# Kernel optimization log

Measured on AMD Instinct MI355X. Metric: run time of the kernel, lower is better.

Reference implementation:

```python
import jax, jax.numpy as jnp
import numpy as np

B, N, S = 8, 512, 96
SD = TD = H = 256
NH, HD = 8, 32  # num_heads, head_dim
OUT = 4


def setup_inputs() -> dict:
    key = jax.random.key(0)
    ks = jax.random.split(key, 20)
    g = lambda k, shape: (jax.random.normal(k, shape, dtype=jnp.float32) * 0.02)
    return {
        "spatial_features": jax.random.normal(ks[0], (B, N, SD), dtype=jnp.float32),
        "temporal_features": jax.random.normal(ks[1], (B, S, TD), dtype=jnp.float32),
        "Ws": g(ks[2], (H, SD)),   "bs": g(ks[3], (H,)),
        "Wt": g(ks[4], (H, TD)),   "bt": g(ks[5], (H,)),
        "Win": g(ks[6], (3 * H, H)), "bin": g(ks[7], (3 * H,)),
        "Wao": g(ks[8], (H, H)),   "bao": g(ks[9], (H,)),
        "W1": g(ks[10], (H, H)),   "b1": g(ks[11], (H,)),
        "Wo1": g(ks[12], (H // 2, H)), "bo1": g(ks[13], (H // 2,)),
        "Wo2": g(ks[14], (OUT, H // 2)), "bo2": g(ks[15], (OUT,)),
    }


def reference(spatial_features, temporal_features, Ws, bs, Wt, bt, Win, bin, Wao, bao,
              W1, b1, Wo1, bo1, Wo2, bo2):
    # Projections
    sp = spatial_features @ Ws.T + bs          # [B, N, H]
    tp = temporal_features @ Wt.T + bt         # [B, S, H]
    # MultiheadAttention in_proj (batched over all N node-queries at once;
    # mathematically identical to the original per-node loop)
    Wq, Wk, Wv = Win[:H], Win[H:2 * H], Win[2 * H:]
    bq, bk, bv = bin[:H], bin[H:2 * H], bin[2 * H:]
    q = (sp @ Wq.T + bq).reshape(B, N, NH, HD)   # [B, N, h, d]
    k = (tp @ Wk.T + bk).reshape(B, S, NH, HD)   # [B, S, h, d]
    v = (tp @ Wv.T + bv).reshape(B, S, NH, HD)
    scale = 1.0 / np.sqrt(HD).astype(np.float32)
    logits = jnp.einsum('bnhd,bshd->bhns', q * scale, k)   # [B, h, N, S]
    attn = jax.nn.softmax(logits, axis=-1)
    ctx = jnp.einsum('bhns,bshd->bnhd', attn, v).reshape(B, N, H)
    attended = ctx @ Wao.T + bao               # [B, N, H] (out_proj)
    # fusion_layer: Linear + ReLU (dropout=identity in eval)
    fused = jax.nn.relu(attended @ W1.T + b1)  # [B, N, H]
    # output_layer: Linear -> ReLU -> Linear
    h2 = jax.nn.relu(fused @ Wo1.T + bo1)      # [B, N, H/2]
    y = h2 @ Wo2.T + bo2                       # [B, N, OUT]
    # original expands over seq_len BEFORE fusion_layer; since all layers are
    # pointwise over the (S, N) grid, compute once per node and broadcast.
    return jnp.broadcast_to(y[:, None, :, :], (B, S, N, OUT))
```

## Files before the change

### kernel.cpp

```cpp
#include <hip/hip_runtime.h>

#define BB 8
#define NN 512
#define SS 96
#define HH 256
#define NHD 8
#define HDD 32
#define OUTD 4

#define Q_OFF   0
#define K_OFF   (4096*256)
#define V_OFF   (K_OFF + 768*256)
#define CTX_OFF (V_OFF + 768*256)
#define BF_BASE (CTX_OFF + 4096*256)
#define WSB_OFF  0
#define WTB_OFF  65536
#define WINB_OFF 131072
#define WAOB_OFF 327680
#define W1B_OFF  393216
#define WO1B_OFF 458752
#define BF_TOTAL 491520

typedef __attribute__((ext_vector_type(8))) short bf16x8;
typedef __attribute__((ext_vector_type(4))) float f32x4;

__device__ __forceinline__ unsigned short f2bf(float f) {
    unsigned int u = __float_as_uint(f);
    u = (u + 0x7FFFu + ((u >> 16) & 1u)) >> 16;
    return (unsigned short)u;
}

__global__ __launch_bounds__(256) void k_cast(
    const float* __restrict__ Ws, const float* __restrict__ Wt,
    const float* __restrict__ Win, const float* __restrict__ Wao,
    const float* __restrict__ W1, const float* __restrict__ Wo1,
    unsigned short* __restrict__ dst)
{
    int idx = blockIdx.x * 256 + threadIdx.x;
    for (int j4 = idx; j4 < BF_TOTAL / 4; j4 += 120 * 256) {
        int e = j4 * 4;
        const float* src; int off;
        if (e < 65536)       { src = Ws;  off = e; }
        else if (e < 131072) { src = Wt;  off = e - 65536; }
        else if (e < 327680) { src = Win; off = e - 131072; }
        else if (e < 393216) { src = Wao; off = e - 327680; }
        else if (e < 458752) { src = W1;  off = e - 393216; }
        else                 { src = Wo1; off = e - 458752; }
        float4 v = *(const float4*)(src + off);
        ushort4 o;
        o.x = f2bf(v.x); o.y = f2bf(v.y); o.z = f2bf(v.z); o.w = f2bf(v.w);
        *(ushort4*)(dst + e) = o;
    }
}

template<int NCT>
__device__ __forceinline__ void mfma_stage(
    const unsigned short* __restrict__ Asw,
    const unsigned short* __restrict__ Wb,
    int lane, int wave, f32x4 acc[NCT])
{
    const int row = lane & 15, kq = lane >> 4;
    #pragma unroll
    for (int ct = 0; ct < NCT; ++ct) acc[ct] = (f32x4){0.f, 0.f, 0.f, 0.f};
    #pragma unroll 2
    for (int kt = 0; kt < 8; ++kt) {
        const int slot = kt * 4 + kq;
        bf16x8 a = *(const bf16x8*)(Asw + row * 256 + ((slot ^ (row & 7)) << 3));
        #pragma unroll
        for (int ct = 0; ct < NCT; ++ct) {
            const unsigned short* wp =
                Wb + (size_t)((wave * NCT + ct) * 16 + row) * 256 + kt * 32 + kq * 8;
            bf16x8 b = *(const bf16x8*)wp;
            acc[ct] = __builtin_amdgcn_mfma_f32_16x16x32_bf16(a, b, acc[ct], 0, 0, 0);
        }
    }
}

template<int NCT, bool RELU>
__device__ __forceinline__ void epi_lds(
    unsigned short* __restrict__ OutSw, const float* __restrict__ bias,
    int lane, int wave, const f32x4 acc[NCT])
{
    const int col0 = lane & 15, rq = lane >> 4;
    #pragma unroll
    for (int ct = 0; ct < NCT; ++ct) {
        const int C = wave * NCT * 16 + ct * 16 + col0;
        const float bb = bias[C];
        const int slot = C >> 3, within = C & 7;
        #pragma unroll
        for (int r = 0; r < 4; ++r) {
            const int R = rq * 4 + r;
            float v = acc[ct][r] + bb;
            if (RELU) v = fmaxf(v, 0.f);
            OutSw[R * 256 + ((slot ^ (R & 7)) << 3) + within] = f2bf(v);
        }
    }
}

template<int NCT>
__device__ __forceinline__ void epi_global(
    float* __restrict__ Og, const float* __restrict__ bias,
    int lane, int wave, const f32x4 acc[NCT])
{
    const int col0 = lane & 15, rq = lane >> 4;
    #pragma unroll
    for (int ct = 0; ct < NCT; ++ct) {
        const int C = wave * NCT * 16 + ct * 16 + col0;
        const float bb = bias[C];
        #pragma unroll
        for (int r = 0; r < 4; ++r) {
            const int R = rq * 4 + r;
            Og[(size_t)R * 256 + C] = acc[ct][r] + bb;
        }
    }
}

__device__ __forceinline__ void stage_A(
    const float* __restrict__ Ag, unsigned short* __restrict__ Asw, int tid)
{
    #pragma unroll
    for (int ii = 0; ii < 4; ++ii) {
        int i = tid + ii * 256;
        int row = i >> 6, c4 = i & 63;
        float4 v = ((const float4*)(Ag + (size_t)row * 256))[c4];
        int col = c4 * 4;
        int slot = col >> 3, half = (col >> 2) & 1;
        ushort4 o;
        o.x = f2bf(v.x); o.y = f2bf(v.y); o.z = f2bf(v.z); o.w = f2bf(v.w);
        *(ushort4*)(Asw + row * 256 + ((slot ^ (row & 7)) << 3) + half * 4) = o;
    }
}

__global__ __launch_bounds__(256) void k_proj(
    const float* __restrict__ spatial, const float* __restrict__ temporal,
    const float* __restrict__ bs, const float* __restrict__ bt,
    const float* __restrict__ bin,
    const unsigned short* __restrict__ bfw,
    float* __restrict__ q_out, float* __restrict__ k_out, float* __restrict__ v_out)
{
    __shared__ __align__(16) unsigned short A0[16 * 256];
    __shared__ __align__(16) unsigned short MID[16 * 256];
    const int tid = threadIdx.x, lane = tid & 63, wave = tid >> 6;
    f32x4 acc[4];

    if (blockIdx.x < 256) {
        const int r0 = blockIdx.x * 16;
        stage_A(spatial + (size_t)r0 * 256, A0, tid);
        __syncthreads();
        mfma_stage<4>(A0, bfw + WSB_OFF, lane, wave, acc);
        epi_lds<4, false>(MID, bs, lane, wave, acc);
        __syncthreads();
        mfma_stage<4>(MID, bfw + WINB_OFF, lane, wave, acc);
        epi_global<4>(q_out + (size_t)r0 * 256, bin, lane, wave, acc);
    } else {
        const int r0 = (blockIdx.x - 256) * 16;
        stage_A(temporal + (size_t)r0 * 256, A0, tid);
        __syncthreads();
        mfma_stage<4>(A0, bfw + WTB_OFF, lane, wave, acc);
        epi_lds<4, false>(MID, bt, lane, wave, acc);
        __syncthreads();
        mfma_stage<4>(MID, bfw + WINB_OFF + 65536, lane, wave, acc);
        epi_global<4>(k_out + (size_t)r0 * 256, bin + 256, lane, wave, acc);
        mfma_stage<4>(MID, bfw + WINB_OFF + 131072, lane, wave, acc);
        epi_global<4>(v_out + (size_t)r0 * 256, bin + 512, lane, wave, acc);
    }
}

__global__ __launch_bounds__(256) void k_attn(
    const float* __restrict__ qg, const float* __restrict__ kg,
    const float* __restrict__ vg, float* __restrict__ ctxg)
{
    __shared__ __align__(16) float kl[SS][HDD];
    __shared__ __align__(16) float vl[SS][HDD];
    const int tid = threadIdx.x;
    const int blk = blockIdx.x;
    const int cc = blk & 3;
    const int h = (blk >> 2) & (NHD - 1);
    const int b = blk >> 5;

    for (int i = tid; i < SS * HDD / 4; i += 256) {
        int s = i >> 3, d4 = i & 7;
        ((float4*)kl[s])[d4] = *(const float4*)(kg + (size_t)(b * SS + s) * HH + h * HDD + d4 * 4);
        ((float4*)vl[s])[d4] = *(const float4*)(vg + (size_t)(b * SS + s) * HH + h * HDD + d4 * 4);
    }
    __syncthreads();

    const int hf = tid & 1;
    const int r = tid >> 1;
    const int n = cc * 128 + r;
    const float4* q4 = (const float4*)(qg + (size_t)(b * NN + n) * HH + h * HDD);
    float4 q[8];
    #pragma unroll
    for (int i = 0; i < 8; ++i) q[i] = q4[i];

    const float scale = 0.17677669529663687f;
    float sum = 0.f;
    float4 ctx[8] = {};
    const int s0 = hf * 48;
    for (int s = s0; s < s0 + 48; ++s) {
        float dot = 0.f;
        #pragma unroll
        for (int i = 0; i < 8; ++i) {
            float4 kk = ((const float4*)kl[s])[i];
            dot += q[i].x * kk.x + q[i].y * kk.y + q[i].z * kk.z + q[i].w * kk.w;
        }
        float p = __expf(dot * scale);
        sum += p;
        #pragma unroll
        for (int i = 0; i < 8; ++i) {
            float4 vv = ((const float4*)vl[s])[i];
            ctx[i].x += p * vv.x; ctx[i].y += p * vv.y;
            ctx[i].z += p * vv.z; ctx[i].w += p * vv.w;
        }
    }
    sum += __shfl_xor(sum, 1);
    #pragma unroll
    for (int i = 0; i < 8; ++i) {
        ctx[i].x += __shfl_xor(ctx[i].x, 1);
        ctx[i].y += __shfl_xor(ctx[i].y, 1);
        ctx[i].z += __shfl_xor(ctx[i].z, 1);
        ctx[i].w += __shfl_xor(ctx[i].w, 1);
    }
    float inv = 1.0f / sum;
    float4* o4 = (float4*)(ctxg + (size_t)(b * NN + n) * HH + h * HDD);
    #pragma unroll
    for (int i = 0; i < 4; ++i) {
        int idx = hf * 4 + i;
        o4[idx] = make_float4(ctx[idx].x * inv, ctx[idx].y * inv,
                              ctx[idx].z * inv, ctx[idx].w * inv);
    }
}

__global__ __launch_bounds__(256) void k_head(
    const float* __restrict__ ctxg,
    const float* __restrict__ bao, const float* __restrict__ b1,
    const float* __restrict__ bo1,
    const float* __restrict__ Wo2, const float* __restrict__ bo2,
    const unsigned short* __restrict__ bfw,
    float* __restrict__ out)
{
    __shared__ __align__(16) unsigned short A0[16 * 256];
    __shared__ __align__(16) unsigned short MID[16 * 256];
    __shared__ __align__(16) float H2[16 * 128];
    __shared__ __align__(16) float y[16][OUTD];
    const int tid = threadIdx.x, lane = tid & 63, wave = tid >> 6;
    const int r0 = blockIdx.x * 16;
    f32x4 acc[4];

    stage_A(ctxg + (size_t)r0 * 256, A0, tid);
    __syncthreads();
    mfma_stage<4>(A0, bfw + WAOB_OFF, lane, wave, acc);
    epi_lds<4, false>(MID, bao, lane, wave, acc);
    __syncthreads();
    mfma_stage<4>(MID, bfw + W1B_OFF, lane, wave, acc);
    epi_lds<4, true>(A0, b1, lane, wave, acc);
    __syncthreads();
    {
        f32x4 a2[2];
        mfma_stage<2>(A0, bfw + WO1B_OFF, lane, wave, a2);
        const int col0 = lane & 15, rq = lane >> 4;
        #pragma unroll
        for (int ct = 0; ct < 2; ++ct) {
            const int C = wave * 32 + ct * 16 + col0;
            const float bb = bo1[C];
            #pragma unroll
            for (int r = 0; r < 4; ++r) {
                const int R = rq * 4 + r;
                H2[R * 128 + C] = fmaxf(a2[ct][r] + bb, 0.f);
            }
        }
    }
    __syncthreads();
    if (tid < 64) {
        int r = tid >> 2, o = tid & 3;
        float a = 0.f;
        const float4* w4 = (const float4*)(Wo2 + (size_t)o * 128);
        const float4* h4 = (const float4*)(H2 + r * 128);
        for (int kk = 0; kk < 32; ++kk) {
            float4 w = w4[kk], hv = h4[kk];
            a += hv.x * w.x + hv.y * w.y + hv.z * w.z + hv.w * w.w;
        }
        y[r][o] = a + bo2[o];
    }
    __syncthreads();
    const int b = r0 >> 9;
    const int nbase = r0 & 511;
    for (int i = tid; i < 16 * SS; i += 256) {
        int s = i >> 4;
        int r = i & 15;
        *(float4*)(out + ((size_t)(b * SS + s) * NN + (nbase + r)) * OUTD) = *(const float4*)y[r];
    }
}

extern "C" void kernel_launch(void* const* d_in, const int* in_sizes, int n_in,
                              void* d_out, int out_size, void* d_ws, size_t ws_size,
                              hipStream_t stream) {
    const float* spatial  = (const float*)d_in[0];
    const float* temporal = (const float*)d_in[1];
    const float* Ws  = (const float*)d_in[2];
    const float* bs  = (const float*)d_in[3];
    const float* Wt  = (const float*)d_in[4];
    const float* bt  = (const float*)d_in[5];
    const float* Win = (const float*)d_in[6];
    const float* bin = (const float*)d_in[7];
    const float* Wao = (const float*)d_in[8];
    const float* bao = (const float*)d_in[9];
    const float* W1  = (const float*)d_in[10];
    const float* b1  = (const float*)d_in[11];
    const float* Wo1 = (const float*)d_in[12];
    const float* bo1 = (const float*)d_in[13];
    const float* Wo2 = (const float*)d_in[14];
    const float* bo2 = (const float*)d_in[15];
    float* out = (float*)d_out;
    float* ws  = (float*)d_ws;

    float* qbuf   = ws + Q_OFF;
    float* kbuf   = ws + K_OFF;
    float* vbuf   = ws + V_OFF;
    float* ctxbuf = ws + CTX_OFF;
    unsigned short* bfw = (unsigned short*)(ws + BF_BASE);

    hipLaunchKernelGGL(k_cast, dim3(120), dim3(256), 0, stream,
                       Ws, Wt, Win, Wao, W1, Wo1, bfw);
    hipLaunchKernelGGL(k_proj, dim3(304), dim3(256), 0, stream,
                       spatial, temporal, bs, bt, bin, bfw, qbuf, kbuf, vbuf);
    hipLaunchKernelGGL(k_attn, dim3(BB * NHD * 4), dim3(256), 0, stream,
                       qbuf, kbuf, vbuf, ctxbuf);
    hipLaunchKernelGGL(k_head, dim3(BB * NN / 16), dim3(256), 0, stream,
                       ctxbuf, bao, b1, bo1, Wo2, bo2, bfw, out);
}
```

Baseline: 152.1 us.

## Fuse attention into head kernel with bf16 MFMA and bf16 Q/K/V^T buffers

Q, K and a transposed V are now stored as bf16 instead of fp32. The scalar fp32 attention kernel is replaced by MFMA-based logits and P·V computed inside the head kernel, so the context never goes to global memory and one launch is removed. This cuts memory traffic and moves the attention math onto the matrix cores. In exchange, probabilities and context are rounded to bf16, which costs some accuracy. Each block now handles all heads for 16 nodes, and the grid drops to 256 blocks.

```diff
diff --git a/kernel.cpp b/kernel.cpp
--- a/kernel.cpp
+++ b/kernel.cpp
@@ -8,11 +8,6 @@
 #define HDD 32
 #define OUTD 4
 
-#define Q_OFF   0
-#define K_OFF   (4096*256)
-#define V_OFF   (K_OFF + 768*256)
-#define CTX_OFF (V_OFF + 768*256)
-#define BF_BASE (CTX_OFF + 4096*256)
 #define WSB_OFF  0
 #define WTB_OFF  65536
 #define WINB_OFF 131072
@@ -20,6 +15,9 @@
 #define W1B_OFF  393216
 #define WO1B_OFF 458752
 #define BF_TOTAL 491520
+#define QB_OFF   491520
+#define KB_OFF   (QB_OFF + 1048576)
+#define VTB_OFF  (KB_OFF + 196608)
 
 typedef __attribute__((ext_vector_type(8))) short bf16x8;
 typedef __attribute__((ext_vector_type(4))) float f32x4;
@@ -98,8 +96,8 @@
 }
 
 template<int NCT>
-__device__ __forceinline__ void epi_global(
-    float* __restrict__ Og, const float* __restrict__ bias,
+__device__ __forceinline__ void epi_gbf16(
+    unsigned short* __restrict__ Og, const float* __restrict__ bias,
     int lane, int wave, const f32x4 acc[NCT])
 {
     const int col0 = lane & 15, rq = lane >> 4;
@@ -110,7 +108,7 @@
         #pragma unroll
         for (int r = 0; r < 4; ++r) {
             const int R = rq * 4 + r;
-            Og[(size_t)R * 256 + C] = acc[ct][r] + bb;
+            Og[(size_t)R * 256 + C] = f2bf(acc[ct][r] + bb);
         }
     }
 }
@@ -131,12 +129,13 @@
     }
 }
 
-__global__ __launch_bounds__(256) void k_proj(
+__global__ __launch_bounds__(256) void k_qkv(
     const float* __restrict__ spatial, const float* __restrict__ temporal,
     const float* __restrict__ bs, const float* __restrict__ bt,
     const float* __restrict__ bin,
     const unsigned short* __restrict__ bfw,
-    float* __restrict__ q_out, float* __restrict__ k_out, float* __restrict__ v_out)
+    unsigned short* __restrict__ qb, unsigned short* __restrict__ kb,
+    unsigned short* __restrict__ vtb)
 {
     __shared__ __align__(16) unsigned short A0[16 * 256];
     __shared__ __align__(16) unsigned short MID[16 * 256];
@@ -151,7 +150,7 @@
         epi_lds<4, false>(MID, bs, lane, wave, acc);
         __syncthreads();
         mfma_stage<4>(MID, bfw + WINB_OFF, lane, wave, acc);
-        epi_global<4>(q_out + (size_t)r0 * 256, bin, lane, wave, acc);
+        epi_gbf16<4>(qb + (size_t)r0 * 256, bin, lane, wave, acc);
     } else {
         const int r0 = (blockIdx.x - 256) * 16;
         stage_A(temporal + (size_t)r0 * 256, A0, tid);
@@ -160,95 +159,100 @@
         epi_lds<4, false>(MID, bt, lane, wave, acc);
         __syncthreads();
         mfma_stage<4>(MID, bfw + WINB_OFF + 65536, lane, wave, acc);
-        epi_global<4>(k_out + (size_t)r0 * 256, bin + 256, lane, wave, acc);
+        epi_gbf16<4>(kb + (size_t)r0 * 256, bin + 256, lane, wave, acc);
         mfma_stage<4>(MID, bfw + WINB_OFF + 131072, lane, wave, acc);
-        epi_global<4>(v_out + (size_t)r0 * 256, bin + 512, lane, wave, acc);
-    }
-}
-
-__global__ __launch_bounds__(256) void k_attn(
-    const float* __restrict__ qg, const float* __restrict__ kg,
-    const float* __restrict__ vg, float* __restrict__ ctxg)
-{
-    __shared__ __align__(16) float kl[SS][HDD];
-    __shared__ __align__(16) float vl[SS][HDD];
-    const int tid = threadIdx.x;
-    const int blk = blockIdx.x;
-    const int cc = blk & 3;
-    const int h = (blk >> 2) & (NHD - 1);
-    const int b = blk >> 5;
-
-    for (int i = tid; i < SS * HDD / 4; i += 256) {
-        int s = i >> 3, d4 = i & 7;
-        ((float4*)kl[s])[d4] = *(const float4*)(kg + (size_t)(b * SS + s) * HH + h * HDD + d4 * 4);
-        ((float4*)vl[s])[d4] = *(const float4*)(vg + (size_t)(b * SS + s) * HH + h * HDD + d4 * 4);
-    }
-    __syncthreads();
-
-    const int hf = tid & 1;
-    const int r = tid >> 1;
-    const int n = cc * 128 + r;
-    const float4* q4 = (const float4*)(qg + (size_t)(b * NN + n) * HH + h * HDD);
-    float4 q[8];
-    #pragma unroll
-    for (int i = 0; i < 8; ++i) q[i] = q4[i];
-
-    const float scale = 0.17677669529663687f;
-    float sum = 0.f;
-    float4 ctx[8] = {};
-    const int s0 = hf * 48;
-    for (int s = s0; s < s0 + 48; ++s) {
-        float dot = 0.f;
-        #pragma unroll
-        for (int i = 0; i < 8; ++i) {
-            float4 kk = ((const float4*)kl[s])[i];
-            dot += q[i].x * kk.x + q[i].y * kk.y + q[i].z * kk.z + q[i].w * kk.w;
-        }
-        float p = __expf(dot * scale);
-        sum += p;
-        #pragma unroll
-        for (int i = 0; i < 8; ++i) {
-            float4 vv = ((const float4*)vl[s])[i];
-            ctx[i].x += p * vv.x; ctx[i].y += p * vv.y;
-            ctx[i].z += p * vv.z; ctx[i].w += p * vv.w;
-        }
-    }
-    sum += __shfl_xor(sum, 1);
-    #pragma unroll
-    for (int i = 0; i < 8; ++i) {
-        ctx[i].x += __shfl_xor(ctx[i].x, 1);
-        ctx[i].y += __shfl_xor(ctx[i].y, 1);
-        ctx[i].z += __shfl_xor(ctx[i].z, 1);
-        ctx[i].w += __shfl_xor(ctx[i].w, 1);
-    }
-    float inv = 1.0f / sum;
-    float4* o4 = (float4*)(ctxg + (size_t)(b * NN + n) * HH + h * HDD);
-    #pragma unroll
-    for (int i = 0; i < 4; ++i) {
-        int idx = hf * 4 + i;
-        o4[idx] = make_float4(ctx[idx].x * inv, ctx[idx].y * inv,
-                              ctx[idx].z * inv, ctx[idx].w * inv);
-    }
-}
-
-__global__ __launch_bounds__(256) void k_head(
-    const float* __restrict__ ctxg,
+        {
+            const int bb_ = r0 / 96, s0 = r0 % 96;
+            const int col0 = lane & 15, rq = lane >> 4;
+            #pragma unroll
+            for (int ct = 0; ct < 4; ++ct) {
+                const int C = wave * 64 + ct * 16 + col0;
+                const float bv = bin[512 + C];
+                #pragma unroll
+                for (int r = 0; r < 4; ++r) {
+                    const int R = rq * 4 + r;
+                    vtb[((size_t)(bb_ * 256 + C)) * 96 + s0 + R] = f2bf(acc[ct][r] + bv);
+                }
+            }
+        }
+    }
+}
+
+__global__ __launch_bounds__(256) void k_attnhead(
+    const unsigned short* __restrict__ qb, const unsigned short* __restrict__ kb,
+    const unsigned short* __restrict__ vtb, const unsigned short* __restrict__ bfw,
     const float* __restrict__ bao, const float* __restrict__ b1,
     const float* __restrict__ bo1,
     const float* __restrict__ Wo2, const float* __restrict__ bo2,
-    const unsigned short* __restrict__ bfw,
     float* __restrict__ out)
 {
     __shared__ __align__(16) unsigned short A0[16 * 256];
     __shared__ __align__(16) unsigned short MID[16 * 256];
     __shared__ __align__(16) float H2[16 * 128];
+    __shared__ __align__(16) unsigned short P[4][16 * 104];
     __shared__ __align__(16) float y[16][OUTD];
     const int tid = threadIdx.x, lane = tid & 63, wave = tid >> 6;
-    const int r0 = blockIdx.x * 16;
+    const int b = blockIdx.x >> 5;
+    const int n0 = (blockIdx.x & 31) * 16;
+    const int cl = lane & 15, kq = lane >> 4;
+    const float scale = 0.17677669529663687f;
+
+    unsigned short* Pw = &P[wave][0];
+    #pragma unroll
+    for (int hh = 0; hh < 2; ++hh) {
+        const int h = wave * 2 + hh;
+        bf16x8 aq = *(const bf16x8*)(qb + (size_t)(b * NN + n0 + cl) * 256 + h * 32 + kq * 8);
+        f32x4 l[6];
+        #pragma unroll
+        for (int t = 0; t < 6; ++t) {
+            bf16x8 bk = *(const bf16x8*)(kb + (size_t)(b * SS + t * 16 + cl) * 256 + h * 32 + kq * 8);
+            l[t] = __builtin_amdgcn_mfma_f32_16x16x32_bf16(aq, bk, (f32x4){0.f,0.f,0.f,0.f}, 0, 0, 0);
+        }
+        float pr[6][4];
+        float sum[4] = {0.f, 0.f, 0.f, 0.f};
+        #pragma unroll
+        for (int t = 0; t < 6; ++t)
+            #pragma unroll
+            for (int r = 0; r < 4; ++r) {
+                float p = __expf(l[t][r] * scale);
+                pr[t][r] = p; sum[r] += p;
+            }
+        #pragma unroll
+        for (int r = 0; r < 4; ++r) {
+            float s = sum[r];
+            s += __shfl_xor(s, 1); s += __shfl_xor(s, 2);
+            s += __shfl_xor(s, 4); s += __shfl_xor(s, 8);
+            sum[r] = 1.0f / s;
+        }
+        #pragma unroll
+        for (int t = 0; t < 6; ++t)
+            #pragma unroll
+            for (int r = 0; r < 4; ++r)
+                Pw[(kq * 4 + r) * 104 + t * 16 + cl] = f2bf(pr[t][r] * sum[r]);
+        f32x4 c0 = (f32x4){0.f,0.f,0.f,0.f}, c1 = (f32x4){0.f,0.f,0.f,0.f};
+        #pragma unroll
+        for (int ks = 0; ks < 3; ++ks) {
+            bf16x8 pa = *(const bf16x8*)(Pw + cl * 104 + ks * 32 + kq * 8);
+            bf16x8 v0 = *(const bf16x8*)(vtb + (size_t)(b * 256 + h * 32 + cl) * 96 + ks * 32 + kq * 8);
+            bf16x8 v1 = *(const bf16x8*)(vtb + (size_t)(b * 256 + h * 32 + 16 + cl) * 96 + ks * 32 + kq * 8);
+            c0 = __builtin_amdgcn_mfma_f32_16x16x32_bf16(pa, v0, c0, 0, 0, 0);
+            c1 = __builtin_amdgcn_mfma_f32_16x16x32_bf16(pa, v1, c1, 0, 0, 0);
+        }
+        #pragma unroll
+        for (int dt = 0; dt < 2; ++dt) {
+            const f32x4 cc = dt ? c1 : c0;
+            const int C = h * 32 + dt * 16 + cl;
+            const int slot = C >> 3, within = C & 7;
+            #pragma unroll
+            for (int r = 0; r < 4; ++r) {
+                const int R = kq * 4 + r;
+                A0[R * 256 + ((slot ^ (R & 7)) << 3) + within] = f2bf(cc[r]);
+            }
+        }
+    }
+    __syncthreads();
+
     f32x4 acc[4];
-
-    stage_A(ctxg + (size_t)r0 * 256, A0, tid);
-    __syncthreads();
     mfma_stage<4>(A0, bfw + WAOB_OFF, lane, wave, acc);
     epi_lds<4, false>(MID, bao, lane, wave, acc);
     __syncthreads();
@@ -258,10 +262,10 @@
     {
         f32x4 a2[2];
         mfma_stage<2>(A0, bfw + WO1B_OFF, lane, wave, a2);
-        const int col0 = lane & 15, rq = lane >> 4;
+        const int rq = lane >> 4;
         #pragma unroll
         for (int ct = 0; ct < 2; ++ct) {
-            const int C = wave * 32 + ct * 16 + col0;
+            const int C = wave * 32 + ct * 16 + cl;
             const float bb = bo1[C];
             #pragma unroll
             for (int r = 0; r < 4; ++r) {
@@ -283,8 +287,7 @@
         y[r][o] = a + bo2[o];
     }
     __syncthreads();
-    const int b = r0 >> 9;
-    const int nbase = r0 & 511;
+    const int nbase = n0;
     for (int i = tid; i < 16 * SS; i += 256) {
         int s = i >> 4;
         int r = i & 15;
@@ -312,20 +315,17 @@
     const float* Wo2 = (const float*)d_in[14];
     const float* bo2 = (const float*)d_in[15];
     float* out = (float*)d_out;
-    float* ws  = (float*)d_ws;
-
-    float* qbuf   = ws + Q_OFF;
-    float* kbuf   = ws + K_OFF;
-    float* vbuf   = ws + V_OFF;
-    float* ctxbuf = ws + CTX_OFF;
-    unsigned short* bfw = (unsigned short*)(ws + BF_BASE);
+    unsigned short* wsu = (unsigned short*)d_ws;
+
+    unsigned short* bfw = wsu;
+    unsigned short* qb  = wsu + QB_OFF;
+    unsigned short* kb  = wsu + KB_OFF;
+    unsigned short* vtb = wsu + VTB_OFF;
 
     hipLaunchKernelGGL(k_cast, dim3(120), dim3(256), 0, stream,
                        Ws, Wt, Win, Wao, W1, Wo1, bfw);
-    hipLaunchKernelGGL(k_proj, dim3(304), dim3(256), 0, stream,
-                       spatial, temporal, bs, bt, bin, bfw, qbuf, kbuf, vbuf);
-    hipLaunchKernelGGL(k_attn, dim3(BB * NHD * 4), dim3(256), 0, stream,
-                       qbuf, kbuf, vbuf, ctxbuf);
-    hipLaunchKernelGGL(k_head, dim3(BB * NN / 16), dim3(256), 0, stream,
-                       ctxbuf, bao, b1, bo1, Wo2, bo2, bfw, out);
-}
+    hipLaunchKernelGGL(k_qkv, dim3(304), dim3(256), 0, stream,
+                       spatial, temporal, bs, bt, bin, bfw, qb, kb, vtb);
+    hipLaunchKernelGGL(k_attnhead, dim3(256), dim3(256), 0, stream,
+                       qb, kb, vtb, bfw, bao, b1, bo1, Wo2, bo2, out);
+}
```

New measurement: 127.1 us. -16.4%, faster.
